# Performance work log

Hardware: AMD Instinct MI355X
Metric: run time of the kernel (lower is better)

The kernel has to match this reference:

```python
import jax, jax.numpy as jnp
import numpy as np

B, S, D, H = 4, 2048, 1024, 16
HEAD = D // H
DENOM = float(np.sqrt(D))  # NOTE: original divides by sqrt(hidden_size), not sqrt(head_size)


def setup_inputs() -> dict:
    key = jax.random.key(0)
    ks = jax.random.split(key, 5)
    scale = 1.0 / np.sqrt(D)
    return {
        "hidden_state": jax.random.normal(ks[0], (B, S, D), dtype=jnp.float32),
        "attention_mask": jnp.ones((B, S), dtype=jnp.int32),  # unused in forward (faithful to source)
        "w_q": jax.random.normal(ks[1], (D, D), dtype=jnp.float32) * scale,
        "w_k": jax.random.normal(ks[2], (D, D), dtype=jnp.float32) * scale,
        "w_v": jax.random.normal(ks[3], (D, D), dtype=jnp.float32) * scale,
        "w_o": jax.random.normal(ks[4], (D, D), dtype=jnp.float32) * scale,
    }


def _split_heads(x):
    # [B, S, D] -> [B, H, S, head]
    b, s, _ = x.shape
    return x.reshape(b, s, H, HEAD).transpose(0, 2, 1, 3)


def reference(hidden_state, attention_mask, w_q, w_k, w_v, w_o):
    # nn.Linear(bias=False): y = x @ W^T with W of shape [out, in]
    q = _split_heads(hidden_state @ w_q.T)  # [B, H, S, head]
    k = _split_heads(hidden_state @ w_k.T)
    v = _split_heads(hidden_state @ w_v.T)
    qk = jnp.einsum("bhqd,bhkd->bhqk", q, k) / DENOM  # scale = 1/sqrt(hidden_size)
    attn = jax.nn.softmax(qk, axis=-1)  # attention_mask is NOT applied (matches source)
    ctx = jnp.einsum("bhqk,bhkd->bhqd", attn, v)  # [B, H, S, head]
    ctx = ctx.transpose(0, 2, 1, 3).reshape(hidden_state.shape[0], hidden_state.shape[1], D)
    return ctx @ w_o.T
```

## Files before the change

### kernel.cpp

```cpp
#include <hip/hip_runtime.h>
#include <hip/hip_bf16.h>
#include <math.h>

typedef __bf16 bf16x8 __attribute__((ext_vector_type(8)));
typedef __bf16 bf16x2 __attribute__((ext_vector_type(2)));
typedef float f32x4 __attribute__((ext_vector_type(4)));
typedef float f32x16 __attribute__((ext_vector_type(16)));
typedef unsigned u32x2v __attribute__((ext_vector_type(2)));
typedef unsigned u32x4v __attribute__((ext_vector_type(4)));
typedef unsigned short u16;

#define QSCALE 0.04508422002778011f

__device__ __forceinline__ u16 f2b(float f) {
  union { float f; unsigned u; } x; x.f = f;
  unsigned r = x.u + 0x7fffu + ((x.u >> 16) & 1u);
  return (u16)(r >> 16);
}

__device__ __forceinline__ unsigned pkbf(float a, float b) {
  bf16x2 t = { (__bf16)a, (__bf16)b };
  return __builtin_bit_cast(unsigned, t);
}

#define GLOAD_LDS16(g, s)                                                      \
  __builtin_amdgcn_global_load_lds(                                            \
      (__attribute__((address_space(1))) void*)(void*)(g),                     \
      (__attribute__((address_space(3))) void*)(s), 16, 0, 0)

#define VMCNT8 asm volatile("s_waitcnt vmcnt(8)" ::: "memory")
#define VMCNT4 asm volatile("s_waitcnt vmcnt(4)" ::: "memory")
#define VMCNT0 asm volatile("s_waitcnt vmcnt(0)" ::: "memory")
#define WAITL  asm volatile("s_waitcnt lgkmcnt(0)" ::: "memory")
#define SBAR   __builtin_amdgcn_s_barrier()

__global__ void cast_bf16_kernel(const float* __restrict__ in, u16* __restrict__ out,
                                 int n4) {
  int i = blockIdx.x * blockDim.x + threadIdx.x;
  int stride = gridDim.x * blockDim.x;
  for (; i < n4; i += stride) {
    float4 v = ((const float4*)in)[i];
    ushort4 o;
    o.x = f2b(v.x); o.y = f2b(v.y); o.z = f2b(v.z); o.w = f2b(v.w);
    ((ushort4*)out)[i] = o;
  }
}

__global__ void cast_w4_kernel(const float* __restrict__ wq, const float* __restrict__ wk,
                               const float* __restrict__ wv, const float* __restrict__ wo,
                               u16* __restrict__ wqkv, u16* __restrict__ wob) {
  const int w = blockIdx.y;
  const float* src = (w == 0) ? wq : (w == 1) ? wk : (w == 2) ? wv : wo;
  u16* dst = (w < 3) ? wqkv + (size_t)w * 1024 * 1024 : wob;
  const float scale = (w == 0) ? QSCALE : 1.0f;
  const int n4 = 1024 * 1024 / 4;
  int i = blockIdx.x * blockDim.x + threadIdx.x;
  int stride = gridDim.x * blockDim.x;
  for (; i < n4; i += stride) {
    float4 v = ((const float4*)src)[i];
    ushort4 o;
    o.x = f2b(v.x * scale); o.y = f2b(v.y * scale);
    o.z = f2b(v.z * scale); o.w = f2b(v.w * scale);
    ((ushort4*)dst)[i] = o;
  }
}

__global__ __launch_bounds__(256) void gemm_qkv(const u16* __restrict__ A,
                                                const u16* __restrict__ Bw,
                                                u16* __restrict__ Qo,
                                                u16* __restrict__ Ko,
                                                u16* __restrict__ Vt) {
  __shared__ u16 As[128 * 32];
  __shared__ u16 Bs[128 * 32];
  const int tid = threadIdx.x;
  const int wid = tid >> 6, lane = tid & 63;
  const int fr = lane & 15, fg = lane >> 4;
  const int wr = wid >> 1, wc = wid & 1;
  const int m0 = blockIdx.y * 128, n0 = blockIdx.x * 128;
  const int K = 1024;

  f32x4 acc[4][4] = {};

  for (int kt = 0; kt < K; kt += 32) {
#pragma unroll
    for (int i2 = 0; i2 < 2; ++i2) {
      int c = i2 * 256 + tid;
      int row = c >> 2, kc = c & 3;
      GLOAD_LDS16(A + (size_t)(m0 + row) * K + kt + kc * 8, (char*)As + c * 16);
      GLOAD_LDS16(Bw + (size_t)(n0 + row) * K + kt + kc * 8, (char*)Bs + c * 16);
    }
    __syncthreads();

    bf16x8 af[4], bfr[4];
#pragma unroll
    for (int m = 0; m < 4; ++m)
      af[m] = *(const bf16x8*)((const char*)As + (wr * 64 + m * 16 + fr) * 64 + fg * 16);
#pragma unroll
    for (int n = 0; n < 4; ++n)
      bfr[n] = *(const bf16x8*)((const char*)Bs + (wc * 64 + n * 16 + fr) * 64 + fg * 16);
#pragma unroll
    for (int m = 0; m < 4; ++m)
#pragma unroll
      for (int n = 0; n < 4; ++n)
        acc[m][n] = __builtin_amdgcn_mfma_f32_16x16x32_bf16(af[m], bfr[n], acc[m][n], 0, 0, 0);
    __syncthreads();
  }

  const int region = n0 >> 10;
#pragma unroll
  for (int m = 0; m < 4; ++m)
#pragma unroll
    for (int n = 0; n < 4; ++n) {
      int gr = m0 + wr * 64 + m * 16 + fg * 4;
      int gc = n0 + wc * 64 + n * 16 + fr;
      if (region == 2) {
        int vc = gc - 2048;
        int hh = vc >> 6, d = vc & 63, bb = gr >> 11, s0 = gr & 2047;
        ushort4 o;
        o.x = f2b(acc[m][n][0]); o.y = f2b(acc[m][n][1]);
        o.z = f2b(acc[m][n][2]); o.w = f2b(acc[m][n][3]);
        *(ushort4*)(Vt + (((size_t)bb * 16 + hh) * 64 + d) * 2048 + s0) = o;
      } else {
        u16* dst = (region == 0) ? Qo : Ko;
        int cc = gc & 1023;
#pragma unroll
        for (int j = 0; j < 4; ++j)
          dst[(size_t)(gr + j) * 1024 + cc] = f2b(acc[m][n][j]);
      }
    }
}

__global__ __launch_bounds__(256) void gemm_o(const u16* __restrict__ A,
                                              const u16* __restrict__ B,
                                              float* __restrict__ Cout) {
  __shared__ u16 As[128 * 32];
  __shared__ u16 Bs[128 * 32];
  const int tid = threadIdx.x;
  const int wid = tid >> 6, lane = tid & 63;
  const int fr = lane & 15, fg = lane >> 4;
  const int wr = wid >> 1, wc = wid & 1;
  const int m0 = blockIdx.y * 128, n0 = blockIdx.x * 128;
  const int K = 1024, N = 1024;

  f32x4 acc[4][4] = {};

  for (int kt = 0; kt < K; kt += 32) {
#pragma unroll
    for (int i2 = 0; i2 < 2; ++i2) {
      int c = i2 * 256 + tid;
      int row = c >> 2, kc = c & 3;
      GLOAD_LDS16(A + (size_t)(m0 + row) * K + kt + kc * 8, (char*)As + c * 16);
      GLOAD_LDS16(B + (size_t)(n0 + row) * K + kt + kc * 8, (char*)Bs + c * 16);
    }
    __syncthreads();

    bf16x8 af[4], bfr[4];
#pragma unroll
    for (int m = 0; m < 4; ++m)
      af[m] = *(const bf16x8*)((const char*)As + (wr * 64 + m * 16 + fr) * 64 + fg * 16);
#pragma unroll
    for (int n = 0; n < 4; ++n)
      bfr[n] = *(const bf16x8*)((const char*)Bs + (wc * 64 + n * 16 + fr) * 64 + fg * 16);
#pragma unroll
    for (int m = 0; m < 4; ++m)
#pragma unroll
      for (int n = 0; n < 4; ++n)
        acc[m][n] = __builtin_amdgcn_mfma_f32_16x16x32_bf16(af[m], bfr[n], acc[m][n], 0, 0, 0);
    __syncthreads();
  }

#pragma unroll
  for (int m = 0; m < 4; ++m)
#pragma unroll
    for (int n = 0; n < 4; ++n) {
      int gr = m0 + wr * 64 + m * 16 + fg * 4;
      int gc = n0 + wc * 64 + n * 16 + fr;
#pragma unroll
      for (int j = 0; j < 4; ++j)
        Cout[(size_t)(gr + j) * 1024 + gc] = acc[m][n][j];
    }
}

__global__ __launch_bounds__(256, 2) void attn_fwd(const u16* __restrict__ Q,
                                                   const u16* __restrict__ Kg,
                                                   const u16* __restrict__ Vtg,
                                                   u16* __restrict__ O) {
  __shared__ u16 Ks[3 * 64 * 64];
  __shared__ u16 Vs[3 * 64 * 64];
  const int tid = threadIdx.x;
  const int wid = tid >> 6, lane = tid & 63;
  const int lq = lane & 31, hi = lane >> 5;
  const int id = blockIdx.x;
  const int swz = (id & 7) * 64 + (id >> 3);
  const int qb = swz & 7, bh = swz >> 3;
  const int b = bh >> 4, h = bh & 15;
  const size_t tokBase = (size_t)b * 2048 * 1024 + h * 64;
  const size_t vBase = (size_t)bh * 64 * 2048;
  const int q0 = qb * 256 + wid * 64;

  bf16x8 qfA[4], qfB[4];
#pragma unroll
  for (int s = 0; s < 4; ++s) {
    qfA[s] = *(const bf16x8*)(Q + tokBase + (size_t)(q0 + lq) * 1024 + s * 16 + hi * 8);
    qfB[s] = *(const bf16x8*)(Q + tokBase + (size_t)(q0 + 32 + lq) * 1024 + s * 16 + hi * 8);
  }

  const bf16x8 ones8 = { (__bf16)1.f, (__bf16)1.f, (__bf16)1.f, (__bf16)1.f,
                         (__bf16)1.f, (__bf16)1.f, (__bf16)1.f, (__bf16)1.f };

  f32x16 accA0 = {}, accA1 = {}, accB0 = {}, accB1 = {};
  f32x16 acclA = {}, acclB = {};

  const int skey = tid >> 3, sdc = tid & 7;
  const int sdg = sdc ^ (skey & 7);
  const int skey2 = (tid + 256) >> 3;
  const int sdg2 = sdc ^ (skey2 & 7);

#define STAGE(off_, k0_) do {                                                         \
    GLOAD_LDS16(Kg + tokBase + (size_t)((k0_) + skey) * 1024 + sdg * 8,               \
                (char*)Ks + (off_) + tid * 16);                                       \
    GLOAD_LDS16(Kg + tokBase + (size_t)((k0_) + skey2) * 1024 + sdg2 * 8,             \
                (char*)Ks + (off_) + (tid + 256) * 16);                               \
    GLOAD_LDS16(Vtg + vBase + (size_t)skey * 2048 + (k0_) + sdg * 8,                  \
                (char*)Vs + (off_) + tid * 16);                                       \
    GLOAD_LDS16(Vtg + vBase + (size_t)skey2 * 2048 + (k0_) + sdg2 * 8,                \
                (char*)Vs + (off_) + (tid + 256) * 16);                               \
  } while (0)

#define TILE(bo_) do {                                                                \
    const char* Kb_ = (const char*)Ks + (bo_);                                        \
    const char* Vb_ = (const char*)Vs + (bo_);                                        \
    f32x16 svA0 = {}, svA1 = {}, svB0 = {}, svB1 = {};                                \
    __builtin_amdgcn_s_setprio(1);                                                    \
    _Pragma("unroll") for (int s = 0; s < 4; ++s) {                                   \
      bf16x8 kf0 = *(const bf16x8*)(Kb_ + lq * 128 +                                  \
                                    ((s * 32 + hi * 16) ^ ((lq & 7) << 4)));          \
      bf16x8 kf1 = *(const bf16x8*)(Kb_ + (32 + lq) * 128 +                           \
                                    ((s * 32 + hi * 16) ^ ((lq & 7) << 4)));          \
      svA0 = __builtin_amdgcn_mfma_f32_32x32x16_bf16(kf0, qfA[s], svA0, 0, 0, 0);     \
      svB0 = __builtin_amdgcn_mfma_f32_32x32x16_bf16(kf0, qfB[s], svB0, 0, 0, 0);     \
      svA1 = __builtin_amdgcn_mfma_f32_32x32x16_bf16(kf1, qfA[s], svA1, 0, 0, 0);     \
      svB1 = __builtin_amdgcn_mfma_f32_32x32x16_bf16(kf1, qfB[s], svB1, 0, 0, 0);     \
    }                                                                                 \
    __builtin_amdgcn_s_setprio(0);                                                    \
    _Pragma("unroll") for (int i = 0; i < 16; ++i)                                    \
      svA0[i] = __builtin_amdgcn_exp2f(svA0[i]);                                      \
    _Pragma("unroll") for (int i = 0; i < 16; ++i)                                    \
      svA1[i] = __builtin_amdgcn_exp2f(svA1[i]);                                      \
    _Pragma("unroll") for (int i = 0; i < 16; ++i)                                    \
      svB0[i] = __builtin_amdgcn_exp2f(svB0[i]);                                      \
    _Pragma("unroll") for (int i = 0; i < 16; ++i)                                    \
      svB1[i] = __builtin_amdgcn_exp2f(svB1[i]);                                      \
    bf16x8 paA[4], paB[4];                                                            \
    _Pragma("unroll") for (int kb = 0; kb < 2; ++kb) {                                \
      _Pragma("unroll") for (int hh = 0; hh < 2; ++hh) {                              \
        const int rb = hh * 8;                                                        \
        {                                                                             \
          const f32x16& pv = kb ? svA1 : svA0;                                        \
          unsigned w01 = pkbf(pv[rb + 0], pv[rb + 1]);                                \
          unsigned w23 = pkbf(pv[rb + 2], pv[rb + 3]);                                \
          unsigned w45 = pkbf(pv[rb + 4], pv[rb + 5]);                                \
          unsigned w67 = pkbf(pv[rb + 6], pv[rb + 7]);                                \
          u32x2v ra = __builtin_amdgcn_permlane32_swap(w01, w45, false, false);       \
          u32x2v rc = __builtin_amdgcn_permlane32_swap(w23, w67, false, false);       \
          u32x4v fw = { ra[0], rc[0], ra[1], rc[1] };                                 \
          paA[kb * 2 + hh] = __builtin_bit_cast(bf16x8, fw);                          \
        }                                                                             \
        {                                                                             \
          const f32x16& pv = kb ? svB1 : svB0;                                        \
          unsigned w01 = pkbf(pv[rb + 0], pv[rb + 1]);                                \
          unsigned w23 = pkbf(pv[rb + 2], pv[rb + 3]);                                \
          unsigned w45 = pkbf(pv[rb + 4], pv[rb + 5]);                                \
          unsigned w67 = pkbf(pv[rb + 6], pv[rb + 7]);                                \
          u32x2v ra = __builtin_amdgcn_permlane32_swap(w01, w45, false, false);       \
          u32x2v rc = __builtin_amdgcn_permlane32_swap(w23, w67, false, false);       \
          u32x4v fw = { ra[0], rc[0], ra[1], rc[1] };                                 \
          paB[kb * 2 + hh] = __builtin_bit_cast(bf16x8, fw);                          \
        }                                                                             \
      }                                                                               \
    }                                                                                 \
    __builtin_amdgcn_s_setprio(1);                                                    \
    _Pragma("unroll") for (int s = 0; s < 4; ++s) {                                   \
      bf16x8 bv0 = *(const bf16x8*)(Vb_ + lq * 128 +                                  \
                                    ((s * 32 + hi * 16) ^ ((lq & 7) << 4)));          \
      bf16x8 bv1 = *(const bf16x8*)(Vb_ + (32 + lq) * 128 +                           \
                                    ((s * 32 + hi * 16) ^ ((lq & 7) << 4)));          \
      accA0 = __builtin_amdgcn_mfma_f32_32x32x16_bf16(paA[s], bv0, accA0, 0, 0, 0);   \
      accA1 = __builtin_amdgcn_mfma_f32_32x32x16_bf16(paA[s], bv1, accA1, 0, 0, 0);   \
      accB0 = __builtin_amdgcn_mfma_f32_32x32x16_bf16(paB[s], bv0, accB0, 0, 0, 0);   \
      accB1 = __builtin_amdgcn_mfma_f32_32x32x16_bf16(paB[s], bv1, accB1, 0, 0, 0);   \
      acclA = __builtin_amdgcn_mfma_f32_32x32x16_bf16(paA[s], ones8, acclA, 0, 0, 0); \
      acclB = __builtin_amdgcn_mfma_f32_32x32x16_bf16(paB[s], ones8, acclB, 0, 0, 0); \
    }                                                                                 \
    __builtin_amdgcn_s_setprio(0);                                                    \
  } while (0)

  STAGE(0, 0);
  STAGE(8192, 64);

  int bo = 0, so = 16384;
  for (int t = 0; t < 30; ++t) {
    STAGE(so, (t + 2) * 64);
    VMCNT8;
    SBAR;
    TILE(bo);
    WAITL;
    SBAR;
    bo += 8192; if (bo == 24576) bo = 0;
    so += 8192; if (so == 24576) so = 0;
  }
  VMCNT4; SBAR;
  TILE(0);
  WAITL; SBAR;
  VMCNT0; SBAR;
  TILE(8192);
#undef TILE
#undef STAGE

#pragma unroll
  for (int r = 0; r < 16; ++r) {
    const int q = (r & 3) + 8 * (r >> 2) + 4 * hi;
    const float ivA = 1.0f / acclA[r];
    const float ivB = 1.0f / acclB[r];
    const size_t rowA = (size_t)(b * 2048 + q0 + q) * 1024 + h * 64;
    const size_t rowB = (size_t)(b * 2048 + q0 + 32 + q) * 1024 + h * 64;
    O[rowA + lq]      = f2b(accA0[r] * ivA);
    O[rowA + 32 + lq] = f2b(accA1[r] * ivA);
    O[rowB + lq]      = f2b(accB0[r] * ivB);
    O[rowB + 32 + lq] = f2b(accB1[r] * ivB);
  }
}

extern "C" void kernel_launch(void* const* d_in, const int* in_sizes, int n_in,
                              void* d_out, int out_size, void* d_ws, size_t ws_size,
                              hipStream_t stream) {
  const float* hs = (const float*)d_in[0];
  const float* wq = (const float*)d_in[2];
  const float* wk = (const float*)d_in[3];
  const float* wv = (const float*)d_in[4];
  const float* wo = (const float*)d_in[5];

  const size_t TOK = 8192, DD = 1024;
  u16* hsb  = (u16*)d_ws;
  u16* wqkv = hsb + TOK * DD;
  u16* wob  = wqkv + 3 * DD * DD;
  u16* Qb   = wob + DD * DD;
  u16* Kb   = Qb + TOK * DD;
  u16* Vtg  = Kb + TOK * DD;
  u16* Cb   = Vtg + TOK * DD;

  cast_bf16_kernel<<<2048, 256, 0, stream>>>(hs, hsb, (int)(TOK * DD / 4));
  cast_w4_kernel<<<dim3(128, 4), 256, 0, stream>>>(wq, wk, wv, wo, wqkv, wob);

  gemm_qkv<<<dim3(24, 64), 256, 0, stream>>>(hsb, wqkv, Qb, Kb, Vtg);

  attn_fwd<<<dim3(512), 256, 0, stream>>>(Qb, Kb, Vtg, Cb);

  gemm_o<<<dim3(8, 64), 256, 0, stream>>>(Cb, wob, (float*)d_out);
}
```

Baseline: 201.1 us.

## Replace ones-MFMA row sums with VALU accumulation and use 128-key double buffering

The softmax denominator is now accumulated in fp32 registers by adding the exponentiated score tiles, then reduced with a cross-half shuffle. This removes the two extra MFMAs per k-step that multiplied P by a ones vector. The K/V staging also changes from a 3-deep ring of 64-key tiles with explicit vmcnt waits to a 2-deep double buffer of 128-key tiles synchronized with __syncthreads. That lowers the barrier count but makes load/compute overlap coarser and may force full vmcnt drains at each barrier.

```diff
diff --git a/kernel.cpp b/kernel.cpp
--- a/kernel.cpp
+++ b/kernel.cpp
@@ -27,12 +27,6 @@
   __builtin_amdgcn_global_load_lds(                                            \
       (__attribute__((address_space(1))) void*)(void*)(g),                     \
       (__attribute__((address_space(3))) void*)(s), 16, 0, 0)
-
-#define VMCNT8 asm volatile("s_waitcnt vmcnt(8)" ::: "memory")
-#define VMCNT4 asm volatile("s_waitcnt vmcnt(4)" ::: "memory")
-#define VMCNT0 asm volatile("s_waitcnt vmcnt(0)" ::: "memory")
-#define WAITL  asm volatile("s_waitcnt lgkmcnt(0)" ::: "memory")
-#define SBAR   __builtin_amdgcn_s_barrier()
 
 __global__ void cast_bf16_kernel(const float* __restrict__ in, u16* __restrict__ out,
                                  int n4) {
@@ -185,8 +179,8 @@
                                                    const u16* __restrict__ Kg,
                                                    const u16* __restrict__ Vtg,
                                                    u16* __restrict__ O) {
-  __shared__ u16 Ks[3 * 64 * 64];
-  __shared__ u16 Vs[3 * 64 * 64];
+  __shared__ u16 Ks[2][128 * 64];
+  __shared__ u16 Vs[2][64 * 128];
   const int tid = threadIdx.x;
   const int wid = tid >> 6, lane = tid & 63;
   const int lq = lane & 31, hi = lane >> 5;
@@ -205,37 +199,32 @@
     qfB[s] = *(const bf16x8*)(Q + tokBase + (size_t)(q0 + 32 + lq) * 1024 + s * 16 + hi * 8);
   }
 
-  const bf16x8 ones8 = { (__bf16)1.f, (__bf16)1.f, (__bf16)1.f, (__bf16)1.f,
-                         (__bf16)1.f, (__bf16)1.f, (__bf16)1.f, (__bf16)1.f };
-
   f32x16 accA0 = {}, accA1 = {}, accB0 = {}, accB1 = {};
-  f32x16 acclA = {}, acclB = {};
+  f32x16 lsvA = {}, lsvB = {};
 
   const int skey = tid >> 3, sdc = tid & 7;
-  const int sdg = sdc ^ (skey & 7);
-  const int skey2 = (tid + 256) >> 3;
-  const int sdg2 = sdc ^ (skey2 & 7);
-
-#define STAGE(off_, k0_) do {                                                         \
-    GLOAD_LDS16(Kg + tokBase + (size_t)((k0_) + skey) * 1024 + sdg * 8,               \
-                (char*)Ks + (off_) + tid * 16);                                       \
-    GLOAD_LDS16(Kg + tokBase + (size_t)((k0_) + skey2) * 1024 + sdg2 * 8,             \
-                (char*)Ks + (off_) + (tid + 256) * 16);                               \
-    GLOAD_LDS16(Vtg + vBase + (size_t)skey * 2048 + (k0_) + sdg * 8,                  \
-                (char*)Vs + (off_) + tid * 16);                                       \
-    GLOAD_LDS16(Vtg + vBase + (size_t)skey2 * 2048 + (k0_) + sdg2 * 8,                \
-                (char*)Vs + (off_) + (tid + 256) * 16);                               \
+  const int sdgK = sdc ^ (skey & 7);
+  const int vd = tid >> 4, vhalf = (tid >> 3) & 1;
+  const int vcol = vhalf * 64 + (sdc ^ (vd & 7)) * 8;
+
+#define STAGE(d_, k0_) do {                                                           \
+    _Pragma("unroll") for (int i = 0; i < 4; ++i) {                                   \
+      GLOAD_LDS16(Kg + tokBase + (size_t)((k0_) + skey + 32 * i) * 1024 + sdgK * 8,   \
+                  (char*)Ks[d_] + (tid + 256 * i) * 16);                              \
+      GLOAD_LDS16(Vtg + vBase + (size_t)(vd + 16 * i) * 2048 + (k0_) + vcol,          \
+                  (char*)Vs[d_] + (tid + 256 * i) * 16);                              \
+    }                                                                                 \
   } while (0)
 
-#define TILE(bo_) do {                                                                \
-    const char* Kb_ = (const char*)Ks + (bo_);                                        \
-    const char* Vb_ = (const char*)Vs + (bo_);                                        \
+#define HALF(d_, h_) do {                                                             \
+    const char* Kb_ = (const char*)Ks[d_];                                            \
+    const char* Vb_ = (const char*)Vs[d_];                                            \
     f32x16 svA0 = {}, svA1 = {}, svB0 = {}, svB1 = {};                                \
     __builtin_amdgcn_s_setprio(1);                                                    \
     _Pragma("unroll") for (int s = 0; s < 4; ++s) {                                   \
-      bf16x8 kf0 = *(const bf16x8*)(Kb_ + lq * 128 +                                  \
+      bf16x8 kf0 = *(const bf16x8*)(Kb_ + ((h_) * 64 + lq) * 128 +                    \
                                     ((s * 32 + hi * 16) ^ ((lq & 7) << 4)));          \
-      bf16x8 kf1 = *(const bf16x8*)(Kb_ + (32 + lq) * 128 +                           \
+      bf16x8 kf1 = *(const bf16x8*)(Kb_ + ((h_) * 64 + 32 + lq) * 128 +               \
                                     ((s * 32 + hi * 16) ^ ((lq & 7) << 4)));          \
       svA0 = __builtin_amdgcn_mfma_f32_32x32x16_bf16(kf0, qfA[s], svA0, 0, 0, 0);     \
       svB0 = __builtin_amdgcn_mfma_f32_32x32x16_bf16(kf0, qfB[s], svB0, 0, 0, 0);     \
@@ -251,6 +240,8 @@
       svB0[i] = __builtin_amdgcn_exp2f(svB0[i]);                                      \
     _Pragma("unroll") for (int i = 0; i < 16; ++i)                                    \
       svB1[i] = __builtin_amdgcn_exp2f(svB1[i]);                                      \
+    lsvA += svA0; lsvA += svA1;                                                       \
+    lsvB += svB0; lsvB += svB1;                                                       \
     bf16x8 paA[4], paB[4];                                                            \
     _Pragma("unroll") for (int kb = 0; kb < 2; ++kb) {                                \
       _Pragma("unroll") for (int hh = 0; hh < 2; ++hh) {                              \
@@ -281,47 +272,40 @@
     }                                                                                 \
     __builtin_amdgcn_s_setprio(1);                                                    \
     _Pragma("unroll") for (int s = 0; s < 4; ++s) {                                   \
-      bf16x8 bv0 = *(const bf16x8*)(Vb_ + lq * 128 +                                  \
+      bf16x8 bv0 = *(const bf16x8*)(Vb_ + lq * 256 + (h_) * 128 +                     \
                                     ((s * 32 + hi * 16) ^ ((lq & 7) << 4)));          \
-      bf16x8 bv1 = *(const bf16x8*)(Vb_ + (32 + lq) * 128 +                           \
+      bf16x8 bv1 = *(const bf16x8*)(Vb_ + (32 + lq) * 256 + (h_) * 128 +              \
                                     ((s * 32 + hi * 16) ^ ((lq & 7) << 4)));          \
       accA0 = __builtin_amdgcn_mfma_f32_32x32x16_bf16(paA[s], bv0, accA0, 0, 0, 0);   \
       accA1 = __builtin_amdgcn_mfma_f32_32x32x16_bf16(paA[s], bv1, accA1, 0, 0, 0);   \
       accB0 = __builtin_amdgcn_mfma_f32_32x32x16_bf16(paB[s], bv0, accB0, 0, 0, 0);   \
       accB1 = __builtin_amdgcn_mfma_f32_32x32x16_bf16(paB[s], bv1, accB1, 0, 0, 0);   \
-      acclA = __builtin_amdgcn_mfma_f32_32x32x16_bf16(paA[s], ones8, acclA, 0, 0, 0); \
-      acclB = __builtin_amdgcn_mfma_f32_32x32x16_bf16(paB[s], ones8, acclB, 0, 0, 0); \
     }                                                                                 \
     __builtin_amdgcn_s_setprio(0);                                                    \
   } while (0)
 
   STAGE(0, 0);
-  STAGE(8192, 64);
-
-  int bo = 0, so = 16384;
-  for (int t = 0; t < 30; ++t) {
-    STAGE(so, (t + 2) * 64);
-    VMCNT8;
-    SBAR;
-    TILE(bo);
-    WAITL;
-    SBAR;
-    bo += 8192; if (bo == 24576) bo = 0;
-    so += 8192; if (so == 24576) so = 0;
-  }
-  VMCNT4; SBAR;
-  TILE(0);
-  WAITL; SBAR;
-  VMCNT0; SBAR;
-  TILE(8192);
-#undef TILE
+  for (int t = 0; t < 16; ++t) {
+    const int d = t & 1;
+    __syncthreads();
+    if (t < 15) STAGE(d ^ 1, (t + 1) * 128);
+    HALF(d, 0);
+    HALF(d, 1);
+  }
+#undef HALF
 #undef STAGE
 
+  float totA = 0.f, totB = 0.f;
+#pragma unroll
+  for (int i = 0; i < 16; ++i) { totA += lsvA[i]; totB += lsvB[i]; }
+  totA += __shfl_xor(totA, 32);
+  totB += __shfl_xor(totB, 32);
+  const float invA = 1.0f / totA, invB = 1.0f / totB;
 #pragma unroll
   for (int r = 0; r < 16; ++r) {
     const int q = (r & 3) + 8 * (r >> 2) + 4 * hi;
-    const float ivA = 1.0f / acclA[r];
-    const float ivB = 1.0f / acclB[r];
+    const float ivA = __shfl(invA, q);
+    const float ivB = __shfl(invB, q);
     const size_t rowA = (size_t)(b * 2048 + q0 + q) * 1024 + h * 64;
     const size_t rowB = (size_t)(b * 2048 + q0 + 32 + q) * 1024 + h * 64;
     O[rowA + lq]      = f2b(accA0[r] * ivA);
```

After: 226.5 us. 1.13x slower.
